# Optimization experiments

Hardware: AMD Instinct MI355X
Metric: run time of the kernel (lower is better)

## Reference

```python
import jax, jax.numpy as jnp
import numpy as np

N_NODES = 30000
N_EDGES = 480000
IN_DIM = 256
OUT_DIM = 256
HEADS = 8
HEAD_DIM = OUT_DIM // HEADS
NEG_SLOPE = 0.2
LN_EPS = 1e-5


def setup_inputs() -> dict:
    key = jax.random.key(0)
    ks = jax.random.split(key, 8)
    x = jax.random.normal(ks[0], (N_NODES, IN_DIM), dtype=jnp.float32)
    edge_index = jax.random.randint(ks[1], (2, N_EDGES), 0, N_NODES, dtype=jnp.int64)
    glorot = 1.0 / np.sqrt(IN_DIM)
    W = jax.random.normal(ks[2], (IN_DIM, HEADS * HEAD_DIM), dtype=jnp.float32) * glorot
    att_src = jax.random.normal(ks[3], (HEADS, HEAD_DIM), dtype=jnp.float32) * (1.0 / np.sqrt(HEAD_DIM))
    att_dst = jax.random.normal(ks[4], (HEADS, HEAD_DIM), dtype=jnp.float32) * (1.0 / np.sqrt(HEAD_DIM))
    bias = jnp.zeros((OUT_DIM,), dtype=jnp.float32)
    gamma = jnp.ones((OUT_DIM,), dtype=jnp.float32)
    beta = jnp.zeros((OUT_DIM,), dtype=jnp.float32)
    return {"x": x, "edge_index": edge_index, "W": W, "att_src": att_src,
            "att_dst": att_dst, "bias": bias, "gamma": gamma, "beta": beta}


def reference(x, edge_index, W, att_src, att_dst, bias, gamma, beta):
    N = x.shape[0]
    # per-head linear projection: [N, H, D]
    h = (x @ W).reshape(N, HEADS, HEAD_DIM)
    # PyG GATConv default: add self-loops
    loops = jnp.arange(N, dtype=edge_index.dtype)
    ei = jnp.concatenate([edge_index, jnp.stack([loops, loops])], axis=1)
    src, dst = ei[0], ei[1]
    # node-level attention logits [N, H]
    a_src = jnp.einsum('nhd,hd->nh', h, att_src)
    a_dst = jnp.einsum('nhd,hd->nh', h, att_dst)
    # edge scores + LeakyReLU  [E, H]
    e = a_src[src] + a_dst[dst]
    e = jnp.where(e > 0, e, NEG_SLOPE * e)
    # segment softmax grouped by destination node
    m = jax.ops.segment_max(e, dst, num_segments=N)
    ex = jnp.exp(e - m[dst])
    denom = jax.ops.segment_sum(ex, dst, num_segments=N)
    alpha = ex / denom[dst]
    # scatter-add weighted source messages  [N, H, D]
    out = jax.ops.segment_sum(h[src] * alpha[:, :, None], dst, num_segments=N)
    out = out.reshape(N, OUT_DIM) + bias
    # LayerNorm
    mu = jnp.mean(out, axis=-1, keepdims=True)
    var = jnp.var(out, axis=-1, keepdims=True)
    out = (out - mu) * jax.lax.rsqrt(var + LN_EPS)
    return out * gamma + beta
```

## Files before the change

kernel.cpp:

```cpp
#include <hip/hip_runtime.h>

#define IN_DIM 256
#define OUT_DIM 256
#define HEADS 8
#define HEAD_DIM 32
#define NEG_SLOPE 0.2f
#define LN_EPS 1e-5f
#define LOG2E 1.4426950408889634f
#define BINS 48
#define BSTRIDE 64
#define NPART 8

typedef __attribute__((ext_vector_type(8))) short bf16x8;
typedef __attribute__((ext_vector_type(4))) float f32x4;
typedef __attribute__((ext_vector_type(4))) unsigned short us4;
typedef __attribute__((ext_vector_type(8))) unsigned short us8;

__device__ inline unsigned short f2b(float f) {
  unsigned u = __float_as_uint(f);
  u += 0x7FFF + ((u >> 16) & 1);
  return (unsigned short)(u >> 16);
}
__device__ inline float b2f(unsigned short u) {
  return __uint_as_float(((unsigned)u) << 16);
}

__global__ __launch_bounds__(256) void convert_wt(const float* __restrict__ W,
                                                  unsigned short* __restrict__ Wt,
                                                  int* __restrict__ cursor,
                                                  int* __restrict__ counts, int M) {
  int i = blockIdx.x * 256 + threadIdx.x;
  int k = i >> 8, n = i & 255;
  Wt[n * 256 + k] = f2b(W[i]);
  if (i < M) {
    cursor[i] = 0;
    if (counts) counts[i] = 0;
  }
}

#define BM 128
#define BN 256
#define BK 64

__global__ __launch_bounds__(512) void gemm_bf16(const float* __restrict__ A,
                                                 const unsigned short* __restrict__ Bt,
                                                 unsigned short* __restrict__ C,
                                                 const float* __restrict__ att_src,
                                                 const float* __restrict__ att_dst,
                                                 float* __restrict__ a_srcP,
                                                 float* __restrict__ a_dstP, int M) {
  __shared__ unsigned short As[BM][BK + 8];
  __shared__ unsigned short Bs[BN][BK + 8];

  const int t = threadIdx.x;
  const int lane = t & 63, wid = t >> 6;
  const int wm = wid >> 2, wn = wid & 3;
  const int row0 = blockIdx.y * BM;
  const int lr = lane & 15, lk = lane >> 4;

  f32x4 acc[4][4] = {};

  for (int kk = 0; kk < IN_DIM; kk += BK) {
    __syncthreads();
    {
      int r = t >> 2, q = (t & 3) * 16;
      int gr = row0 + r;
      float4 f0 = make_float4(0, 0, 0, 0), f1 = f0, f2 = f0, f3 = f0;
      if (gr < M) {
        const float4* ap = (const float4*)&A[(size_t)gr * IN_DIM + kk + q];
        f0 = ap[0]; f1 = ap[1]; f2 = ap[2]; f3 = ap[3];
      }
      us8 o0, o1;
      o0[0] = f2b(f0.x); o0[1] = f2b(f0.y); o0[2] = f2b(f0.z); o0[3] = f2b(f0.w);
      o0[4] = f2b(f1.x); o0[5] = f2b(f1.y); o0[6] = f2b(f1.z); o0[7] = f2b(f1.w);
      o1[0] = f2b(f2.x); o1[1] = f2b(f2.y); o1[2] = f2b(f2.z); o1[3] = f2b(f2.w);
      o1[4] = f2b(f3.x); o1[5] = f2b(f3.y); o1[6] = f2b(f3.z); o1[7] = f2b(f3.w);
      *(us8*)&As[r][q] = o0;
      *(us8*)&As[r][q + 8] = o1;
    }
#pragma unroll
    for (int c = t; c < 2048; c += 512) {
      int r = c >> 3, off = (c & 7) * 8;
      us8 v = *(const us8*)&Bt[(size_t)r * IN_DIM + kk + off];
      *(us8*)&Bs[r][off] = v;
    }
    __syncthreads();

#pragma unroll
    for (int ks = 0; ks < 2; ++ks) {
      bf16x8 af[4], bfr[4];
#pragma unroll
      for (int i = 0; i < 4; ++i)
        af[i] = *(bf16x8*)&As[wm * 64 + i * 16 + lr][ks * 32 + lk * 8];
#pragma unroll
      for (int i = 0; i < 4; ++i)
        bfr[i] = *(bf16x8*)&Bs[wn * 64 + i * 16 + lr][ks * 32 + lk * 8];
#pragma unroll
      for (int i = 0; i < 4; ++i)
#pragma unroll
        for (int j = 0; j < 4; ++j)
          acc[i][j] = __builtin_amdgcn_mfma_f32_16x16x32_bf16(af[i], bfr[j], acc[i][j], 0, 0, 0);
    }
  }

#pragma unroll
  for (int i = 0; i < 4; ++i) {
#pragma unroll
    for (int q = 0; q < 4; ++q) {
      int row = row0 + wm * 64 + i * 16 + lk * 4 + q;
      if (row < M) {
#pragma unroll
        for (int j = 0; j < 4; ++j) {
          int col = wn * 64 + j * 16 + lr;
          C[(size_t)row * OUT_DIM + col] = f2b(acc[i][j][q]);
        }
      }
    }
  }

  float att_s[4], att_d[4];
#pragma unroll
  for (int j = 0; j < 4; ++j) {
    int hd = wn * 2 + (j >> 1);
    int dd = (j & 1) * 16 + lr;
    att_s[j] = att_src[hd * HEAD_DIM + dd];
    att_d[j] = att_dst[hd * HEAD_DIM + dd];
  }
#pragma unroll
  for (int i = 0; i < 4; ++i) {
#pragma unroll
    for (int q = 0; q < 4; ++q) {
      float ps0 = acc[i][0][q] * att_s[0] + acc[i][1][q] * att_s[1];
      float ps1 = acc[i][2][q] * att_s[2] + acc[i][3][q] * att_s[3];
      float pd0 = acc[i][0][q] * att_d[0] + acc[i][1][q] * att_d[1];
      float pd1 = acc[i][2][q] * att_d[2] + acc[i][3][q] * att_d[3];
#pragma unroll
      for (int off = 1; off < 16; off <<= 1) {
        ps0 += __shfl_xor(ps0, off);
        ps1 += __shfl_xor(ps1, off);
        pd0 += __shfl_xor(pd0, off);
        pd1 += __shfl_xor(pd1, off);
      }
      int row = row0 + wm * 64 + i * 16 + lk * 4 + q;
      if (lr == 0 && row < M) {
        a_srcP[row * 8 + wn * 2]     = ps0;
        a_srcP[row * 8 + wn * 2 + 1] = ps1;
        a_dstP[row * 8 + wn * 2]     = pd0;
        a_dstP[row * 8 + wn * 2 + 1] = pd1;
      }
    }
  }
}

__global__ __launch_bounds__(256) void scatter_bins(const int* __restrict__ ei,
                                                    int* __restrict__ cursor,
                                                    unsigned short* __restrict__ colb,
                                                    int E, int range) {
  int p = blockIdx.x & (NPART - 1);
  int e = (blockIdx.x >> 3) * 256 + threadIdx.x;
  if (e >= E) return;
  int d = ei[E + e];
  if ((unsigned)(d - p * range) >= (unsigned)range) return;
  int s = ei[e];
  int k = atomicAdd(&cursor[d], 1);
  if (k >= BINS) return;
  colb[d * BSTRIDE + k] = (unsigned short)s;
}

__device__ __forceinline__ void aggregate_body(const unsigned short* hb,
                                               const float* a_src, const float* a_dst,
                                               const unsigned short* col,
                                               const float* bias, const float* gamma,
                                               const float* beta, float* out,
                                               int node, int lane, int beg, int end) {
  int head2 = lane >> 3;

  float adst = a_dst[node * 8 + head2];
  float ls = a_src[node * 8 + head2] + adst;
  ls = (ls > 0.f) ? ls : NEG_SLOPE * ls;
  float ws = exp2f(ls * LOG2E);

  const char* hblane = (const char*)hb + (lane << 3);

  float S = ws;
  float4 acc;
  {
    us4 hv = *(const us4*)(hblane + ((unsigned)node << 9));
    acc.x = ws * b2f(hv[0]); acc.y = ws * b2f(hv[1]);
    acc.z = ws * b2f(hv[2]); acc.w = ws * b2f(hv[3]);
  }

  int e = beg;
  int sP[8];
  bool haveP = (e + 8 <= end);
  if (haveP) {
#pragma unroll
    for (int j = 0; j < 8; ++j) sP[j] = col[e + j];
  }
  while (haveP) {
    int s[8];
#pragma unroll
    for (int j = 0; j < 8; ++j) s[j] = sP[j];
    int en = e + 8;
    haveP = (en + 8 <= end);
    if (haveP) {
#pragma unroll
      for (int j = 0; j < 8; ++j) sP[j] = col[en + j];
    }
    float aV[8];
#pragma unroll
    for (int j = 0; j < 8; ++j)
      aV[j] = a_src[s[j] * 8 + head2];
    us4 v[8];
#pragma unroll
    for (int j = 0; j < 8; ++j)
      v[j] = *(const us4*)(hblane + ((unsigned)s[j] << 9));
#pragma unroll
    for (int j = 0; j < 8; ++j) {
      float l = aV[j] + adst;
      l = (l > 0.f) ? l : NEG_SLOPE * l;
      float w = exp2f(l * LOG2E);
      S += w;
      acc.x += w * b2f(v[j][0]);
      acc.y += w * b2f(v[j][1]);
      acc.z += w * b2f(v[j][2]);
      acc.w += w * b2f(v[j][3]);
    }
    e = en;
  }
  for (; e < end; ++e) {
    int s = col[e];
    float l = a_src[s * 8 + head2] + adst;
    l = (l > 0.f) ? l : NEG_SLOPE * l;
    float w = exp2f(l * LOG2E);
    us4 hv = *(const us4*)(hblane + ((unsigned)s << 9));
    S += w;
    acc.x += w * b2f(hv[0]); acc.y += w * b2f(hv[1]);
    acc.z += w * b2f(hv[2]); acc.w += w * b2f(hv[3]);
  }
  float inv = 1.f / S;
  acc.x *= inv; acc.y *= inv; acc.z *= inv; acc.w *= inv;

  float4 b4 = *(const float4*)&bias[lane * 4];
  acc.x += b4.x; acc.y += b4.y; acc.z += b4.z; acc.w += b4.w;

  float s1 = acc.x + acc.y + acc.z + acc.w;
#pragma unroll
  for (int off = 1; off < 64; off <<= 1) s1 += __shfl_xor(s1, off);
  float mean = s1 * (1.f / OUT_DIM);

  float4 c = make_float4(acc.x - mean, acc.y - mean, acc.z - mean, acc.w - mean);
  float s2v = c.x * c.x + c.y * c.y + c.z * c.z + c.w * c.w;
#pragma unroll
  for (int off = 1; off < 64; off <<= 1) s2v += __shfl_xor(s2v, off);
  float rstd = rsqrtf(s2v * (1.f / OUT_DIM) + LN_EPS);

  float4 g4 = *(const float4*)&gamma[lane * 4];
  float4 e4 = *(const float4*)&beta[lane * 4];
  float4 o;
  o.x = c.x * rstd * g4.x + e4.x;
  o.y = c.y * rstd * g4.y + e4.y;
  o.z = c.z * rstd * g4.z + e4.z;
  o.w = c.w * rstd * g4.w + e4.w;
  *(float4*)&out[(size_t)node * OUT_DIM + lane * 4] = o;
}

__global__ __launch_bounds__(256) void aggregate_bins(const unsigned short* __restrict__ hb,
                                                      const float* __restrict__ a_src,
                                                      const float* __restrict__ a_dst,
                                                      const int* __restrict__ cursor,
                                                      const unsigned short* __restrict__ colb,
                                                      const float* __restrict__ bias,
                                                      const float* __restrict__ gamma,
                                                      const float* __restrict__ beta,
                                                      float* __restrict__ out, int n_nodes) {
  int node = blockIdx.x * 4 + (threadIdx.x >> 6);
  int lane = threadIdx.x & 63;
  if (node >= n_nodes) return;
  int deg = cursor[node];
  deg = (deg < BINS) ? deg : BINS;
  int base = node * BSTRIDE;
  aggregate_body(hb, a_src, a_dst, colb, bias, gamma, beta, out,
                 node, lane, base, base + deg);
}

__global__ __launch_bounds__(256) void count_kernel(const int* __restrict__ ei,
                                                    int* __restrict__ counts, int E) {
  int e = blockIdx.x * 256 + threadIdx.x;
  if (e >= E) return;
  atomicAdd(&counts[ei[E + e]], 1);
}

__global__ __launch_bounds__(256) void block_sums(const int* __restrict__ counts,
                                                  int* __restrict__ bsum, int n) {
  int i = blockIdx.x * 256 + threadIdx.x;
  int lane = threadIdx.x & 63, wid = threadIdx.x >> 6;
  int v = (i < n) ? counts[i] : 0;
#pragma unroll
  for (int off = 1; off < 64; off <<= 1) v += __shfl_xor(v, off);
  __shared__ int ws[4];
  if (lane == 0) ws[wid] = v;
  __syncthreads();
  if (threadIdx.x == 0) bsum[blockIdx.x] = ws[0] + ws[1] + ws[2] + ws[3];
}

__global__ __launch_bounds__(128) void scan_sums(const int* __restrict__ bsum,
                                                 int* __restrict__ bofs, int nb) {
  int t = threadIdx.x, lane = t & 63, wid = t >> 6;
  int v = (t < nb) ? bsum[t] : 0;
  int incl = v;
#pragma unroll
  for (int off = 1; off < 64; off <<= 1) {
    int o = __shfl_up(incl, off);
    if (lane >= off) incl += o;
  }
  __shared__ int ws[2];
  if (lane == 63) ws[wid] = incl;
  __syncthreads();
  if (wid == 1) incl += ws[0];
  if (t < nb) bofs[t] = incl - v;
}

__global__ __launch_bounds__(256) void scan_final(const int* __restrict__ counts,
                                                  const int* __restrict__ bofs,
                                                  int* __restrict__ row_start,
                                                  int* __restrict__ cursor, int n) {
  int i = blockIdx.x * 256 + threadIdx.x;
  int lane = threadIdx.x & 63, wid = threadIdx.x >> 6;
  int v = (i < n) ? counts[i] : 0;
  int incl = v;
#pragma unroll
  for (int off = 1; off < 64; off <<= 1) {
    int o = __shfl_up(incl, off);
    if (lane >= off) incl += o;
  }
  __shared__ int ws[4];
  if (lane == 63) ws[wid] = incl;
  __syncthreads();
  int wadd = 0;
#pragma unroll
  for (int j = 0; j < 4; ++j)
    if (j < wid) wadd += ws[j];
  int excl = bofs[blockIdx.x] + wadd + incl - v;
  if (i < n) { row_start[i] = excl; cursor[i] = excl; }
  if (i == n - 1) row_start[n] = excl + v;
}

__global__ __launch_bounds__(256) void scatter_csr(const int* __restrict__ ei,
                                                   int* __restrict__ cursor,
                                                   unsigned short* __restrict__ col_src, int E) {
  int e = blockIdx.x * 256 + threadIdx.x;
  if (e >= E) return;
  int s = ei[e];
  int d = ei[E + e];
  int pos = atomicAdd(&cursor[d], 1);
  col_src[pos] = (unsigned short)s;
}

__global__ __launch_bounds__(256) void aggregate_csr(const unsigned short* __restrict__ hb,
                                                     const float* __restrict__ a_src,
                                                     const float* __restrict__ a_dst,
                                                     const int* __restrict__ row_start,
                                                     const unsigned short* __restrict__ col_src,
                                                     const float* __restrict__ bias,
                                                     const float* __restrict__ gamma,
                                                     const float* __restrict__ beta,
                                                     float* __restrict__ out, int n_nodes) {
  int node = blockIdx.x * 4 + (threadIdx.x >> 6);
  int lane = threadIdx.x & 63;
  if (node >= n_nodes) return;
  aggregate_body(hb, a_src, a_dst, col_src, bias, gamma, beta, out,
                 node, lane, row_start[node], row_start[node + 1]);
}

extern "C" void kernel_launch(void* const* d_in, const int* in_sizes, int n_in,
                              void* d_out, int out_size, void* d_ws, size_t ws_size,
                              hipStream_t stream) {
  const float* x       = (const float*)d_in[0];
  const int*   ei      = (const int*)d_in[1];
  const float* W       = (const float*)d_in[2];
  const float* att_src = (const float*)d_in[3];
  const float* att_dst = (const float*)d_in[4];
  const float* bias    = (const float*)d_in[5];
  const float* gamma   = (const float*)d_in[6];
  const float* beta    = (const float*)d_in[7];
  float* out = (float*)d_out;

  const int M = in_sizes[0] / IN_DIM;
  const int E = in_sizes[1] / 2;
  const int NB = (M + 255) / 256;

  char* w = (char*)d_ws;
  auto carve = [&](size_t bytes) {
    char* p = w;
    w += (bytes + 255) & ~(size_t)255;
    return p;
  };

  unsigned short* Wt = (unsigned short*)carve((size_t)IN_DIM * OUT_DIM * 2);
  unsigned short* hb = (unsigned short*)carve((size_t)M * OUT_DIM * 2);
  float* a_srcP = (float*)carve((size_t)M * HEADS * 4);
  float* a_dstP = (float*)carve((size_t)M * HEADS * 4);
  int* cursor   = (int*)carve((size_t)M * 4);

  size_t bins_need = (size_t)M * BSTRIDE * 2 + (1 << 20);
  size_t used = (size_t)(w - (char*)d_ws);
  bool use_bins = (ws_size >= used + bins_need);

  if (use_bins) {
    unsigned short* colb = (unsigned short*)carve((size_t)M * BSTRIDE * 2);
    int range = (M + NPART - 1) / NPART;

    convert_wt<<<(IN_DIM * OUT_DIM) / 256, 256, 0, stream>>>(W, Wt, cursor, nullptr, M);
    scatter_bins<<<NPART * ((E + 255) / 256), 256, 0, stream>>>(ei, cursor, colb, E, range);
    gemm_bf16<<<dim3(1, (M + BM - 1) / BM), 512, 0, stream>>>(x, Wt, hb, att_src, att_dst,
                                                              a_srcP, a_dstP, M);
    aggregate_bins<<<(M + 3) / 4, 256, 0, stream>>>(hb, a_srcP, a_dstP, cursor, colb,
                                                    bias, gamma, beta, out, M);
  } else {
    int* row_st  = (int*)carve((size_t)(M + 1) * 4);
    int* counts  = (int*)carve((size_t)M * 4);
    int* bsum    = (int*)carve((size_t)NB * 4);
    int* bofs    = (int*)carve((size_t)NB * 4);
    unsigned short* col_src = (unsigned short*)carve((size_t)E * 2);

    convert_wt<<<(IN_DIM * OUT_DIM) / 256, 256, 0, stream>>>(W, Wt, cursor, counts, M);
    count_kernel<<<(E + 255) / 256, 256, 0, stream>>>(ei, counts, E);
    block_sums<<<NB, 256, 0, stream>>>(counts, bsum, M);
    scan_sums<<<1, 128, 0, stream>>>(bsum, bofs, NB);
    scan_final<<<NB, 256, 0, stream>>>(counts, bofs, row_st, cursor, M);
    scatter_csr<<<(E + 255) / 256, 256, 0, stream>>>(ei, cursor, col_src, E);
    gemm_bf16<<<dim3(1, (M + BM - 1) / BM), 512, 0, stream>>>(x, Wt, hb, att_src, att_dst,
                                                              a_srcP, a_dstP, M);
    aggregate_csr<<<(M + 3) / 4, 256, 0, stream>>>(hb, a_srcP, a_dstP, row_st, col_src,
                                                   bias, gamma, beta, out, M);
  }
}
```

Before: 97.31 us.

## Fuse edge scatter into GEMM launch as extra blocks to overlap work

The separate scatter_bins kernel is removed and its work is appended as extra blocks in the GEMM grid, 64 blocks each striding over an edge chunk for one destination partition. The bandwidth-bound edge binning can then run concurrently with the compute-bound GEMM, and one launch is saved. The cost is far fewer scatter blocks (64 versus about 15000), so each block runs a long serial loop. Partition p is derived from the block index while the chunk comes from sidx, which may leave some chunk/partition pairs misassigned if NGEMM is not a multiple of 8.

```diff
diff --git a/kernel.cpp b/kernel.cpp
--- a/kernel.cpp
+++ b/kernel.cpp
@@ -10,6 +10,7 @@
 #define BINS 48
 #define BSTRIDE 64
 #define NPART 8
+#define SCHUNKS 8
 
 typedef __attribute__((ext_vector_type(8))) short bf16x8;
 typedef __attribute__((ext_vector_type(4))) float f32x4;
@@ -42,20 +43,44 @@
 #define BN 256
 #define BK 64
 
-__global__ __launch_bounds__(512) void gemm_bf16(const float* __restrict__ A,
-                                                 const unsigned short* __restrict__ Bt,
-                                                 unsigned short* __restrict__ C,
-                                                 const float* __restrict__ att_src,
-                                                 const float* __restrict__ att_dst,
-                                                 float* __restrict__ a_srcP,
-                                                 float* __restrict__ a_dstP, int M) {
+__global__ __launch_bounds__(512) void gemm_scatter(const float* __restrict__ A,
+                                                    const unsigned short* __restrict__ Bt,
+                                                    unsigned short* __restrict__ C,
+                                                    const float* __restrict__ att_src,
+                                                    const float* __restrict__ att_dst,
+                                                    float* __restrict__ a_srcP,
+                                                    float* __restrict__ a_dstP,
+                                                    const int* __restrict__ ei,
+                                                    int* __restrict__ cursor,
+                                                    unsigned short* __restrict__ colb,
+                                                    int M, int E, int range, int ngemm) {
+  const int by = blockIdx.y;
+
+  if (by >= ngemm) {
+    int sidx = by - ngemm;
+    int p = by & (NPART - 1);
+    int c = sidx >> 3;
+    int chunk = (E + SCHUNKS - 1) / SCHUNKS;
+    int lo = c * chunk;
+    int hi = min(lo + chunk, E);
+    for (int e = lo + (int)threadIdx.x; e < hi; e += 512) {
+      int d = ei[E + e];
+      if ((unsigned)(d - p * range) >= (unsigned)range) continue;
+      int s = ei[e];
+      int k = atomicAdd(&cursor[d], 1);
+      if (k >= BINS) continue;
+      colb[d * BSTRIDE + k] = (unsigned short)s;
+    }
+    return;
+  }
+
   __shared__ unsigned short As[BM][BK + 8];
   __shared__ unsigned short Bs[BN][BK + 8];
 
   const int t = threadIdx.x;
   const int lane = t & 63, wid = t >> 6;
   const int wm = wid >> 2, wn = wid & 3;
-  const int row0 = blockIdx.y * BM;
+  const int row0 = by * BM;
   const int lr = lane & 15, lk = lane >> 4;
 
   f32x4 acc[4][4] = {};
@@ -152,21 +177,6 @@
   }
 }
 
-__global__ __launch_bounds__(256) void scatter_bins(const int* __restrict__ ei,
-                                                    int* __restrict__ cursor,
-                                                    unsigned short* __restrict__ colb,
-                                                    int E, int range) {
-  int p = blockIdx.x & (NPART - 1);
-  int e = (blockIdx.x >> 3) * 256 + threadIdx.x;
-  if (e >= E) return;
-  int d = ei[E + e];
-  if ((unsigned)(d - p * range) >= (unsigned)range) return;
-  int s = ei[e];
-  int k = atomicAdd(&cursor[d], 1);
-  if (k >= BINS) return;
-  colb[d * BSTRIDE + k] = (unsigned short)s;
-}
-
 __device__ __forceinline__ void aggregate_body(const unsigned short* hb,
                                                const float* a_src, const float* a_dst,
                                                const unsigned short* col,
@@ -389,6 +399,7 @@
   const int M = in_sizes[0] / IN_DIM;
   const int E = in_sizes[1] / 2;
   const int NB = (M + 255) / 256;
+  const int NGEMM = (M + BM - 1) / BM;
 
   char* w = (char*)d_ws;
   auto carve = [&](size_t bytes) {
@@ -412,9 +423,8 @@
     int range = (M + NPART - 1) / NPART;
 
     convert_wt<<<(IN_DIM * OUT_DIM) / 256, 256, 0, stream>>>(W, Wt, cursor, nullptr, M);
-    scatter_bins<<<NPART * ((E + 255) / 256), 256, 0, stream>>>(ei, cursor, colb, E, range);
-    gemm_bf16<<<dim3(1, (M + BM - 1) / BM), 512, 0, stream>>>(x, Wt, hb, att_src, att_dst,
-                                                              a_srcP, a_dstP, M);
+    gemm_scatter<<<dim3(1, NGEMM + NPART * SCHUNKS), 512, 0, stream>>>(
+        x, Wt, hb, att_src, att_dst, a_srcP, a_dstP, ei, cursor, colb, M, E, range, NGEMM);
     aggregate_bins<<<(M + 3) / 4, 256, 0, stream>>>(hb, a_srcP, a_dstP, cursor, colb,
                                                     bias, gamma, beta, out, M);
   } else {
@@ -430,8 +440,8 @@
     scan_sums<<<1, 128, 0, stream>>>(bsum, bofs, NB);
     scan_final<<<NB, 256, 0, stream>>>(counts, bofs, row_st, cursor, M);
     scatter_csr<<<(E + 255) / 256, 256, 0, stream>>>(ei, cursor, col_src, E);
-    gemm_bf16<<<dim3(1, (M + BM - 1) / BM), 512, 0, stream>>>(x, Wt, hb, att_src, att_dst,
-                                                              a_srcP, a_dstP, M);
+    gemm_scatter<<<dim3(1, NGEMM), 512, 0, stream>>>(
+        x, Wt, hb, att_src, att_dst, a_srcP, a_dstP, ei, cursor, nullptr, M, E, M, NGEMM);
     aggregate_csr<<<(M + 3) / 4, 256, 0, stream>>>(hb, a_srcP, a_dstP, row_st, col_src,
                                                    bias, gamma, beta, out, M);
   }
```

Result: slower. 178.0 us (+82.9%).
